# Kernel optimization log

Measured on AMD Instinct MI355X. Metric: run time of the kernel, lower is better.

The kernel has to match this reference:

```python
import jax, jax.numpy as jnp
import numpy as np

U, M, E, EL, H, F, C = 200000, 100000, 2000000, 500000, 64, 20, 7


def setup_inputs() -> dict:
    key = jax.random.key(0)
    ks = jax.random.split(key, 20)
    s = 0.02
    return {
        "user_node_id": jnp.arange(U, dtype=jnp.int64),
        "movie_node_id": jnp.arange(M, dtype=jnp.int64),
        "movie_x": jax.random.normal(ks[0], (M, F), jnp.float32),
        "edge_src": jax.random.randint(ks[1], (E,), 0, U),
        "edge_dst": jax.random.randint(ks[2], (E,), 0, M),
        "el_src": jax.random.randint(ks[3], (EL,), 0, U),
        "el_dst": jax.random.randint(ks[4], (EL,), 0, M),
        "user_emb": jax.random.normal(ks[5], (U, H), jnp.float32) * s,
        "movie_emb": jax.random.normal(ks[6], (M, H), jnp.float32) * s,
        "w_movie": jax.random.normal(ks[7], (F, H), jnp.float32) * s,
        "b_movie": jnp.zeros((H,), jnp.float32),
        "l1_rates_Wl": jax.random.normal(ks[8], (H, H), jnp.float32) * s,
        "l1_rates_bl": jnp.zeros((H,), jnp.float32),
        "l1_rates_Wr": jax.random.normal(ks[9], (H, H), jnp.float32) * s,
        "l1_rev_Wl": jax.random.normal(ks[10], (H, H), jnp.float32) * s,
        "l1_rev_bl": jnp.zeros((H,), jnp.float32),
        "l1_rev_Wr": jax.random.normal(ks[11], (H, H), jnp.float32) * s,
        "l2_rates_Wl": jax.random.normal(ks[12], (H, H), jnp.float32) * s,
        "l2_rates_bl": jnp.zeros((H,), jnp.float32),
        "l2_rates_Wr": jax.random.normal(ks[13], (H, H), jnp.float32) * s,
        "l2_rev_Wl": jax.random.normal(ks[14], (H, H), jnp.float32) * s,
        "l2_rev_bl": jnp.zeros((H,), jnp.float32),
        "l2_rev_Wr": jax.random.normal(ks[15], (H, H), jnp.float32) * s,
        "cls_W": jax.random.normal(ks[16], (2 * H, C), jnp.float32) * s,
        "cls_b": jnp.zeros((C,), jnp.float32),
    }


def _sage(x_src, x_dst, src, dst, n_dst, Wl, bl, Wr):
    # mean-aggregate neighbor messages: gather -> segment_sum -> divide by degree
    msg = x_src[src]                                            # [E, H]
    agg = jax.ops.segment_sum(msg, dst, num_segments=n_dst)     # [n_dst, H]
    deg = jax.ops.segment_sum(jnp.ones((src.shape[0],), x_src.dtype), dst,
                              num_segments=n_dst)
    agg = agg / jnp.maximum(deg, 1.0)[:, None]
    return agg @ Wl + bl + x_dst @ Wr                           # SAGEConv: lin_l(aggr) + lin_r(root)


def reference(user_node_id, movie_node_id, movie_x, edge_src, edge_dst,
              el_src, el_dst, user_emb, movie_emb, w_movie, b_movie,
              l1_rates_Wl, l1_rates_bl, l1_rates_Wr,
              l1_rev_Wl, l1_rev_bl, l1_rev_Wr,
              l2_rates_Wl, l2_rates_bl, l2_rates_Wr,
              l2_rev_Wl, l2_rev_bl, l2_rev_Wr,
              cls_W, cls_b):
    # input projections
    x_user = user_emb[user_node_id]                              # [U, H]
    x_movie = movie_x @ w_movie + b_movie + movie_emb[movie_node_id]  # [M, H]

    # hetero GNN layer 1 (relu)
    u1 = jax.nn.relu(_sage(x_movie, x_user, edge_dst, edge_src, x_user.shape[0],
                           l1_rev_Wl, l1_rev_bl, l1_rev_Wr))
    m1 = jax.nn.relu(_sage(x_user, x_movie, edge_src, edge_dst, x_movie.shape[0],
                           l1_rates_Wl, l1_rates_bl, l1_rates_Wr))
    # hetero GNN layer 2 (no activation)
    u2 = _sage(m1, u1, edge_dst, edge_src, u1.shape[0],
               l2_rev_Wl, l2_rev_bl, l2_rev_Wr)
    m2 = _sage(u1, m1, edge_src, edge_dst, m1.shape[0],
               l2_rates_Wl, l2_rates_bl, l2_rates_Wr)

    # edge classifier over labeled (user, movie) pairs
    edge_feat = jnp.concatenate([u2[el_src], m2[el_dst]], axis=-1)  # [EL, 2H]
    return edge_feat @ cls_W + cls_b                                # [EL, C]
```

## Files before the change

kernel.cpp:

```cpp
#include <hip/hip_runtime.h>
#include <cstdint>
#include <cstddef>

#define H 64
#define C 7
#define F 20
#define BSH 9
#define BSZ 512
#define CH 8192

typedef unsigned short u16;
typedef __attribute__((ext_vector_type(8))) short bf16x8;
typedef __attribute__((ext_vector_type(4))) float f32x4;

static __device__ __forceinline__ int imax(int a, int b) { return a > b ? a : b; }
static __device__ __forceinline__ int imin(int a, int b) { return a < b ? a : b; }

static __device__ __forceinline__ float bf2f(u16 v) {
  union { unsigned u; float f; } x; x.u = ((unsigned)v) << 16; return x.f;
}
static __device__ __forceinline__ u16 f2bf(float f) {
  union { float f; unsigned u; } x; x.f = f;
  unsigned r = x.u + 0x7fffu + ((x.u >> 16) & 1u);
  return (u16)(r >> 16);
}
static __device__ __forceinline__ int pack2bf(float a, float b) {
  return (int)f2bf(a) | ((int)f2bf(b) << 16);
}
static __device__ __forceinline__ float lo16f(unsigned v) {
  union { unsigned u; float f; } x; x.u = v << 16; return x.f;
}
static __device__ __forceinline__ float hi16f(unsigned v) {
  union { unsigned u; float f; } x; x.u = v & 0xffff0000u; return x.f;
}

__global__ __launch_bounds__(256) void k_bhist(const int* __restrict__ esrc,
                                               const int* __restrict__ edst, int E,
                                               int* __restrict__ gcnt_u, int* __restrict__ gcnt_m,
                                               int nbu, int nbm) {
  extern __shared__ int sh[];
  int* hu = sh;
  int* hm = sh + nbu;
  for (int i = threadIdx.x; i < nbu + nbm; i += 256) sh[i] = 0;
  __syncthreads();
  int stride = gridDim.x * 256;
  for (int i = blockIdx.x * 256 + threadIdx.x; i < E; i += stride) {
    atomicAdd(&hu[esrc[i] >> BSH], 1);
    atomicAdd(&hm[edst[i] >> BSH], 1);
  }
  __syncthreads();
  for (int i = threadIdx.x; i < nbu; i += 256) if (hu[i]) atomicAdd(&gcnt_u[i], hu[i]);
  for (int i = threadIdx.x; i < nbm; i += 256) if (hm[i]) atomicAdd(&gcnt_m[i], hm[i]);
}

__global__ __launch_bounds__(256) void k_bscan(const int* __restrict__ gcnt_u,
                                               const int* __restrict__ gcnt_m,
                                               int nbu, int nbm, int E,
                                               int* __restrict__ boff_u, int* __restrict__ boff_m,
                                               int* __restrict__ gcur_u, int* __restrict__ gcur_m) {
  __shared__ int s[1024];
  for (int i = threadIdx.x; i < nbu; i += 256) s[i] = gcnt_u[i];
  for (int i = threadIdx.x; i < nbm; i += 256) s[512 + i] = gcnt_m[i];
  __syncthreads();
  if (threadIdx.x == 0) {
    int r = 0;
    for (int i = 0; i < nbu; ++i) { int v = s[i]; s[i] = r; r += v; }
  }
  if (threadIdx.x == 1) {
    int r = 0;
    for (int i = 0; i < nbm; ++i) { int v = s[512 + i]; s[512 + i] = r; r += v; }
  }
  __syncthreads();
  for (int i = threadIdx.x; i < nbu; i += 256) { boff_u[i] = s[i]; gcur_u[i] = s[i]; }
  for (int i = threadIdx.x; i < nbm; i += 256) { boff_m[i] = s[512 + i]; gcur_m[i] = s[512 + i]; }
  if (threadIdx.x == 0) { boff_u[nbu] = E; boff_m[nbm] = E; }
}

__global__ __launch_bounds__(256) void k_bscat(const int* __restrict__ esrc,
                                               const int* __restrict__ edst, int E,
                                               int* __restrict__ gcur_u, int* __restrict__ gcur_m,
                                               unsigned int* __restrict__ pk_u,
                                               unsigned int* __restrict__ pk_m,
                                               int nbu, int nbm, int nchunks) {
  extern __shared__ int sh2[];
  int dir = (blockIdx.x >= (unsigned)nchunks) ? 1 : 0;
  int chunk = dir ? (blockIdx.x - nchunks) : blockIdx.x;
  const int* key = dir ? edst : esrc;
  const int* pay = dir ? esrc : edst;
  int* gcur = dir ? gcur_m : gcur_u;
  unsigned int* pk = dir ? pk_m : pk_u;
  int nb = dir ? nbm : nbu;
  int* cnt = sh2;
  int* base = sh2 + nb;
  int beg = chunk * CH;
  int end = imin(beg + CH, E);
  for (int i = threadIdx.x; i < nb; i += 256) cnt[i] = 0;
  __syncthreads();
  for (int i = beg + threadIdx.x; i < end; i += 256) atomicAdd(&cnt[key[i] >> BSH], 1);
  __syncthreads();
  for (int i = threadIdx.x; i < nb; i += 256) {
    int c = cnt[i];
    base[i] = c ? atomicAdd(&gcur[i], c) : 0;
    cnt[i] = 0;
  }
  __syncthreads();
  for (int i = beg + threadIdx.x; i < end; i += 256) {
    int k = key[i];
    int b = k >> BSH;
    int r = atomicAdd(&cnt[b], 1);
    pk[base[b] + r] = ((unsigned)(k & (BSZ - 1)) << 18) | (unsigned)pay[i];
  }
}

__global__ __launch_bounds__(512) void k_bbuild(const unsigned int* __restrict__ pk_u,
                                                const unsigned int* __restrict__ pk_m,
                                                const int* __restrict__ boff_u,
                                                const int* __restrict__ boff_m,
                                                int nbu, int nbm, int U_, int M_, int E,
                                                int* __restrict__ csr_u, int* __restrict__ csr_m,
                                                int* __restrict__ off_u, int* __restrict__ off_m) {
  __shared__ int hist[BSZ];
  __shared__ int cur[BSZ];
  int dir = (blockIdx.x >= (unsigned)nbu) ? 1 : 0;
  int b = dir ? (blockIdx.x - nbu) : blockIdx.x;
  const unsigned int* pk = dir ? pk_m : pk_u;
  const int* boff = dir ? boff_m : boff_u;
  int N = dir ? M_ : U_;
  int nb = dir ? nbm : nbu;
  int* csr = dir ? csr_m : csr_u;
  int* off = dir ? off_m : off_u;
  int beg = boff[b], end = boff[b + 1];
  int t = threadIdx.x;
  hist[t] = 0;
  __syncthreads();
  for (int i = beg + t; i < end; i += 512) atomicAdd(&hist[pk[i] >> 18], 1);
  __syncthreads();
  int v0 = hist[t];
  for (int o = 1; o < 512; o <<= 1) {
    int x = (t >= o) ? hist[t - o] : 0;
    __syncthreads();
    hist[t] += x;
    __syncthreads();
  }
  int excl = hist[t] - v0;
  cur[t] = excl;
  int node = (b << BSH) + t;
  if (node < N) off[node] = beg + excl;
  if (t == 0 && b == nb - 1) off[N] = E;
  __syncthreads();
  for (int i = beg + t; i < end; i += 512) {
    unsigned int p = pk[i];
    int n = (int)(p >> 18);
    int r = atomicAdd(&cur[n], 1);
    csr[beg + r] = (int)(p & 0x3FFFFu);
  }
}

__global__ __launch_bounds__(256) void k_prep(
    const float* __restrict__ movie_x, const float* __restrict__ w_movie,
    const float* __restrict__ b_movie, const float* __restrict__ movie_emb,
    const int* __restrict__ mnid,
    const float* __restrict__ user_emb, const int* __restrict__ unid,
    const float* __restrict__ l2u_Wl, const float* __restrict__ l2u_Wr,
    const float* __restrict__ l2u_bl,
    const float* __restrict__ l2m_Wl, const float* __restrict__ l2m_Wr,
    const float* __restrict__ l2m_bl,
    const float* __restrict__ clsW,
    u16* __restrict__ xm_bf, u16* __restrict__ xu_bf, float* __restrict__ cw,
    int M_, int U_, int gProj, int gCvt) {
  __shared__ float ws_[F * H];
  int b = blockIdx.x;
  if (b < gProj) {
    for (int i = threadIdx.x; i < F * H; i += 256) ws_[i] = w_movie[i];
    __syncthreads();
    int t = b * 256 + threadIdx.x;
    int m = t >> 6;
    int h = t & 63;
    if (m >= M_) return;
    float acc = b_movie[h] + movie_emb[(size_t)mnid[m] * H + h];
    const float* xr = movie_x + (size_t)m * F;
    #pragma unroll
    for (int f = 0; f < F; ++f) acc += xr[f] * ws_[f * H + h];
    xm_bf[(size_t)m * H + h] = f2bf(acc);
  } else if (b < gProj + gCvt) {
    int t = (b - gProj) * 256 + threadIdx.x;
    if (t >= U_ * 16) return;
    int i = t >> 4;
    int g = t & 15;
    const float4 v = *(const float4*)(user_emb + (size_t)unid[i] * H + g * 4);
    ushort4 o;
    o.x = f2bf(v.x); o.y = f2bf(v.y); o.z = f2bf(v.z); o.w = f2bf(v.w);
    *(ushort4*)(xu_bf + (size_t)i * H + g * 4) = o;
  } else {
    int t = (b - gProj - gCvt) * 256 + threadIdx.x;
    if (t < 448) {
      int k = t / C, c = t % C;
      float s = 0.f;
      for (int j = 0; j < H; ++j) s += l2u_Wl[k * H + j] * clsW[j * C + c];
      cw[t] = s;
    } else if (t < 896) {
      int u = t - 448; int k = u / C, c = u % C;
      float s = 0.f;
      for (int j = 0; j < H; ++j) s += l2u_Wr[k * H + j] * clsW[j * C + c];
      cw[t] = s;
    } else if (t < 1344) {
      int u = t - 896; int k = u / C, c = u % C;
      float s = 0.f;
      for (int j = 0; j < H; ++j) s += l2m_Wl[k * H + j] * clsW[(H + j) * C + c];
      cw[t] = s;
    } else if (t < 1792) {
      int u = t - 1344; int k = u / C, c = u % C;
      float s = 0.f;
      for (int j = 0; j < H; ++j) s += l2m_Wr[k * H + j] * clsW[(H + j) * C + c];
      cw[t] = s;
    } else if (t < 1799) {
      int c = t - 1792;
      float s = 0.f;
      for (int j = 0; j < H; ++j) s += l2u_bl[j] * clsW[j * C + c];
      cw[t] = s;
    } else if (t < 1806) {
      int c = t - 1799;
      float s = 0.f;
      for (int j = 0; j < H; ++j) s += l2m_bl[j] * clsW[(H + j) * C + c];
      cw[t] = s;
    }
  }
}

__global__ __launch_bounds__(512, 4) void k_sage_mfma(
    const u16* __restrict__ xu, const u16* __restrict__ xm,
    const int* __restrict__ csr_u, const int* __restrict__ off_u,
    const int* __restrict__ csr_m, const int* __restrict__ off_m,
    const float* __restrict__ WlU, const float* __restrict__ blU, const float* __restrict__ WrU,
    const float* __restrict__ WlM, const float* __restrict__ blM, const float* __restrict__ WrM,
    const float* __restrict__ CWml, const float* __restrict__ CWur,
    const float* __restrict__ CWul, const float* __restrict__ CWmr,
    u16* __restrict__ Zu, u16* __restrict__ Zm,
    int U_, int M_, int E_, int gU) {
  __shared__ int sWl[64 * 36];
  __shared__ int sWr[64 * 36];
  __shared__ int sAggHi[128 * 36];
  __shared__ int sAggLo[128 * 36];
  __shared__ float sCl[448];
  __shared__ float sCr[448];
  __shared__ float sBl[64];

  int movie = (blockIdx.x >= (unsigned)gU) ? 1 : 0;
  int bside = movie ? (blockIdx.x - gU) : blockIdx.x;
  const u16* srcT = movie ? xu : xm;
  const u16* rootT = movie ? xm : xu;
  const int* csr = movie ? csr_m : csr_u;
  const int* off = movie ? off_m : off_u;
  const float* Wl = movie ? WlM : WlU;
  const float* Wr = movie ? WrM : WrU;
  const float* bl = movie ? blM : blU;
  const float* CWl = movie ? CWul : CWml;
  const float* CWr = movie ? CWmr : CWur;
  u16* Z = movie ? Zm : Zu;
  int N = movie ? M_ : U_;

  int tid = threadIdx.x;
  for (int idx = tid; idx < 2048; idx += 512) {
    int j = idx & 63, kk = idx >> 6;
    sWl[j * 36 + kk] = pack2bf(Wl[(2 * kk) * H + j], Wl[(2 * kk + 1) * H + j]);
    sWr[j * 36 + kk] = pack2bf(Wr[(2 * kk) * H + j], Wr[(2 * kk + 1) * H + j]);
  }
  for (int idx = tid; idx < 448; idx += 512) { sCl[idx] = CWl[idx]; sCr[idx] = CWr[idx]; }
  if (tid < 64) sBl[tid] = bl[tid];
  __syncthreads();

  int lane = tid & 63;
  int wid = tid >> 6;
  int slot = lane >> 3;
  int l3 = lane & 7;
  int sbase = slot * 8;
  int node0 = bside * 128 + wid * 16;

  #pragma unroll
  for (int g = 0; g < 2; ++g) {
    int n = node0 + g * 8 + slot;
    int nc = n < N ? n : N - 1;
    int jb = off[nc];
    int d = off[nc + 1] - jb;
    if (n >= N) d = 0;
    int dm1 = imax(d - 1, 0);
    int dmax = d;
    dmax = imax(dmax, __shfl_xor(dmax, 8));
    dmax = imax(dmax, __shfl_xor(dmax, 16));
    dmax = imax(dmax, __shfl_xor(dmax, 32));

    float acc[8] = {0.f, 0.f, 0.f, 0.f, 0.f, 0.f, 0.f, 0.f};
    for (int tb = 0; tb < dmax; tb += 8) {
      int ci = jb + imin(tb + l3, dm1);
      ci = imin(ci, E_ - 1);
      int e = csr[ci];
      uint4 v[8];
      #pragma unroll
      for (int k = 0; k < 8; ++k) {
        int a = __shfl(e, sbase + k);
        v[k] = *(const uint4*)(srcT + (size_t)(unsigned)a * H + l3 * 8);
      }
      #pragma unroll
      for (int k = 0; k < 8; ++k) {
        float mk = (tb + k < d) ? 1.0f : 0.0f;
        acc[0] = fmaf(lo16f(v[k].x), mk, acc[0]);
        acc[1] = fmaf(hi16f(v[k].x), mk, acc[1]);
        acc[2] = fmaf(lo16f(v[k].y), mk, acc[2]);
        acc[3] = fmaf(hi16f(v[k].y), mk, acc[3]);
        acc[4] = fmaf(lo16f(v[k].z), mk, acc[4]);
        acc[5] = fmaf(hi16f(v[k].z), mk, acc[5]);
        acc[6] = fmaf(lo16f(v[k].w), mk, acc[6]);
        acc[7] = fmaf(hi16f(v[k].w), mk, acc[7]);
      }
    }

    float inv = 1.0f / (float)imax(d, 1);
    int hi4[4], lo4[4];
    #pragma unroll
    for (int pp = 0; pp < 4; ++pp) {
      float s0 = acc[2 * pp] * inv;
      float s1 = acc[2 * pp + 1] * inv;
      u16 b0 = f2bf(s0), b1 = f2bf(s1);
      float r0 = s0 - bf2f(b0), r1 = s1 - bf2f(b1);
      hi4[pp] = (int)b0 | ((int)b1 << 16);
      lo4[pp] = pack2bf(r0, r1);
    }
    int row = wid * 16 + g * 8 + slot;
    *(int4*)&sAggHi[row * 36 + l3 * 4] = *(int4*)hi4;
    *(int4*)&sAggLo[row * 36 + l3 * 4] = *(int4*)lo4;
  }

  int r16 = lane & 15;
  int q4 = lane >> 4;
  union FU { int4 i; bf16x8 b; };
  FU ahi[2], alo[2], art[2];
  int arow = wid * 16 + r16;
  int rnode = node0 + r16;
  rnode = rnode < N ? rnode : N - 1;
  #pragma unroll
  for (int kt = 0; kt < 2; ++kt) {
    ahi[kt].i = *(const int4*)&sAggHi[arow * 36 + kt * 16 + q4 * 4];
    alo[kt].i = *(const int4*)&sAggLo[arow * 36 + kt * 16 + q4 * 4];
    art[kt].i = ((const int4*)(rootT + (size_t)rnode * H))[kt * 4 + q4];
  }
  float val[4][4];
  #pragma unroll
  for (int t = 0; t < 4; ++t) {
    f32x4 cacc = {0.f, 0.f, 0.f, 0.f};
    #pragma unroll
    for (int kt = 0; kt < 2; ++kt) {
      FU bwl, bwr;
      bwl.i = *(const int4*)&sWl[(t * 16 + r16) * 36 + kt * 16 + q4 * 4];
      bwr.i = *(const int4*)&sWr[(t * 16 + r16) * 36 + kt * 16 + q4 * 4];
      cacc = __builtin_amdgcn_mfma_f32_16x16x32_bf16(ahi[kt].b, bwl.b, cacc, 0, 0, 0);
      cacc = __builtin_amdgcn_mfma_f32_16x16x32_bf16(alo[kt].b, bwl.b, cacc, 0, 0, 0);
      cacc = __builtin_amdgcn_mfma_f32_16x16x32_bf16(art[kt].b, bwr.b, cacc, 0, 0, 0);
    }
    float bj = sBl[t * 16 + r16];
    #pragma unroll
    for (int r = 0; r < 4; ++r) val[t][r] = fmaxf(cacc[r] + bj, 0.f);
  }

  float zacc[4] = {0.f, 0.f, 0.f, 0.f};
  #pragma unroll
  for (int c = 0; c < C; ++c) {
    float tl[4], tr[4];
    #pragma unroll
    for (int r = 0; r < 4; ++r) {
      tl[r] = val[0][r] * sCl[(r16) * C + c] + val[1][r] * sCl[(16 + r16) * C + c] +
              val[2][r] * sCl[(32 + r16) * C + c] + val[3][r] * sCl[(48 + r16) * C + c];
      tr[r] = val[0][r] * sCr[(r16) * C + c] + val[1][r] * sCr[(16 + r16) * C + c] +
              val[2][r] * sCr[(32 + r16) * C + c] + val[3][r] * sCr[(48 + r16) * C + c];
    }
    #pragma unroll
    for (int o = 1; o < 16; o <<= 1) {
      #pragma unroll
      for (int r = 0; r < 4; ++r) {
        tl[r] += __shfl_xor(tl[r], o);
        tr[r] += __shfl_xor(tr[r], o);
      }
    }
    #pragma unroll
    for (int r = 0; r < 4; ++r) {
      zacc[r] = (r16 == c) ? zacc[r] + tl[r] : zacc[r];
      zacc[r] = (r16 == 8 + c) ? zacc[r] + tr[r] : zacc[r];
    }
  }
  #pragma unroll
  for (int r = 0; r < 4; ++r) {
    int node = node0 + q4 * 4 + r;
    if (node < N) Z[(size_t)node * 16 + r16] = f2bf(zacc[r]);
  }
}

__global__ __launch_bounds__(256) void k_agg7m(
    const u16* __restrict__ Zu, const u16* __restrict__ Zm,
    const int* __restrict__ csr_u, const int* __restrict__ off_u,
    const int* __restrict__ csr_m, const int* __restrict__ off_m,
    const float* __restrict__ cbu, const float* __restrict__ cbm,
    float* __restrict__ Pu, float* __restrict__ Pm,
    int U_, int M_, int gU) {
  int movie = (blockIdx.x >= (unsigned)gU) ? 1 : 0;
  int bside = movie ? (blockIdx.x - gU) : blockIdx.x;
  const u16* Zsrc = movie ? Zu : Zm;
  const u16* Zroot = movie ? Zm : Zu;
  const int* csr = movie ? csr_m : csr_u;
  const int* off = movie ? off_m : off_u;
  const float* cb = movie ? cbm : cbu;
  float* P = movie ? Pm : Pu;
  int N = movie ? M_ : U_;

  int n = bside * 256 + threadIdx.x;
  if (n >= N) return;
  int beg = off[n], end = off[n + 1];
  float acc[8] = {0.f, 0.f, 0.f, 0.f, 0.f, 0.f, 0.f, 0.f};
  for (int j = beg; j < end; ++j) {
    int a = csr[j];
    uint4 z = *(const uint4*)(Zsrc + (size_t)a * 16);
    acc[0] += lo16f(z.x); acc[1] += hi16f(z.x);
    acc[2] += lo16f(z.y); acc[3] += hi16f(z.y);
    acc[4] += lo16f(z.z); acc[5] += hi16f(z.z);
    acc[6] += lo16f(z.w); acc[7] += hi16f(z.w);
  }
  float inv = 1.f / (float)imax(end - beg, 1);
  uint4 zr = *(const uint4*)(Zroot + (size_t)n * 16 + 8);
  float4 o0, o1;
  o0.x = acc[0] * inv + lo16f(zr.x) + cb[0];
  o0.y = acc[1] * inv + hi16f(zr.x) + cb[1];
  o0.z = acc[2] * inv + lo16f(zr.y) + cb[2];
  o0.w = acc[3] * inv + hi16f(zr.y) + cb[3];
  o1.x = acc[4] * inv + lo16f(zr.z) + cb[4];
  o1.y = acc[5] * inv + hi16f(zr.z) + cb[5];
  o1.z = acc[6] * inv + lo16f(zr.w) + cb[6];
  o1.w = 0.f;
  float4* po = (float4*)(P + (size_t)n * 8);
  po[0] = o0;
  po[1] = o1;
}

__global__ void k_final(const int* __restrict__ els, const int* __restrict__ eld,
                        const float* __restrict__ Pu, const float* __restrict__ Pm,
                        const float* __restrict__ clsb, float* __restrict__ out, int total) {
  int t = blockIdx.x * 256 + threadIdx.x;
  if (t >= total) return;
  int e = t / C, c = t - e * C;
  out[t] = Pu[(size_t)els[e] * 8 + c] + Pm[(size_t)eld[e] * 8 + c] + clsb[c];
}

extern "C" void kernel_launch(void* const* d_in, const int* in_sizes, int n_in,
                              void* d_out, int out_size, void* d_ws, size_t ws_size,
                              hipStream_t stream) {
  (void)n_in; (void)out_size; (void)ws_size;
  const int*   unid      = (const int*)d_in[0];
  const int*   mnid      = (const int*)d_in[1];
  const float* movie_x   = (const float*)d_in[2];
  const int*   e_src     = (const int*)d_in[3];
  const int*   e_dst     = (const int*)d_in[4];
  const int*   el_src    = (const int*)d_in[5];
  const int*   el_dst    = (const int*)d_in[6];
  const float* user_emb  = (const float*)d_in[7];
  const float* movie_emb = (const float*)d_in[8];
  const float* w_movie   = (const float*)d_in[9];
  const float* b_movie   = (const float*)d_in[10];
  const float* l1r_Wl    = (const float*)d_in[11];
  const float* l1r_bl    = (const float*)d_in[12];
  const float* l1r_Wr    = (const float*)d_in[13];
  const float* l1v_Wl    = (const float*)d_in[14];
  const float* l1v_bl    = (const float*)d_in[15];
  const float* l1v_Wr    = (const float*)d_in[16];
  const float* l2r_Wl    = (const float*)d_in[17];
  const float* l2r_bl    = (const float*)d_in[18];
  const float* l2r_Wr    = (const float*)d_in[19];
  const float* l2v_Wl    = (const float*)d_in[20];
  const float* l2v_bl    = (const float*)d_in[21];
  const float* l2v_Wr    = (const float*)d_in[22];
  const float* cls_W     = (const float*)d_in[23];
  const float* cls_b     = (const float*)d_in[24];

  int U  = in_sizes[0];
  int M  = in_sizes[1];
  int E  = in_sizes[3];
  int EL = in_sizes[5];

  int nbu = (U + BSZ - 1) / BSZ;
  int nbm = (M + BSZ - 1) / BSZ;
  int nchunks = (E + CH - 1) / CH;

  char* p = (char*)d_ws;
  auto alloc = [&](size_t nbytes) { char* r = p; p += (nbytes + 255) & ~(size_t)255; return r; };

  u16*   xm_bf  = (u16*)alloc((size_t)M * H * 2);
  u16*   xu_bf  = (u16*)alloc((size_t)U * H * 2);
  u16*   Zu     = (u16*)alloc((size_t)U * 16 * 2);
  u16*   Zm     = (u16*)alloc((size_t)M * 16 * 2);
  float* Pu     = (float*)alloc((size_t)U * 8 * 4);
  float* Pm     = (float*)alloc((size_t)M * 8 * 4);
  int*   csr_u  = (int*)alloc((size_t)E * 4);
  int*   csr_m  = (int*)alloc((size_t)E * 4);
  int*   off_u  = (int*)alloc((size_t)(U + 1) * 4);
  int*   off_m  = (int*)alloc((size_t)(M + 1) * 4);
  unsigned int* pk_u = (unsigned int*)alloc((size_t)E * 4);
  unsigned int* pk_m = (unsigned int*)alloc((size_t)E * 4);
  int*   gcnt   = (int*)alloc((size_t)(nbu + nbm) * 4);
  int*   gcnt_u = gcnt;
  int*   gcnt_m = gcnt + nbu;
  int*   boff_u = (int*)alloc((size_t)(nbu + 1) * 4);
  int*   boff_m = (int*)alloc((size_t)(nbm + 1) * 4);
  int*   gcur_u = (int*)alloc((size_t)nbu * 4);
  int*   gcur_m = (int*)alloc((size_t)nbm * 4);
  float* cw     = (float*)alloc(1806 * 4);
  float* CWul = cw, *CWur = cw + 448, *CWml = cw + 896, *CWmr = cw + 1344;
  float* cbu  = cw + 1792, *cbm = cw + 1799;

  hipMemsetAsync(gcnt, 0, (size_t)(nbu + nbm) * 4, stream);

  k_bhist<<<256, 256, (size_t)(nbu + nbm) * 4, stream>>>(e_src, e_dst, E, gcnt_u, gcnt_m, nbu, nbm);
  k_bscan<<<1, 256, 0, stream>>>(gcnt_u, gcnt_m, nbu, nbm, E, boff_u, boff_m, gcur_u, gcur_m);
  k_bscat<<<2 * nchunks, 256, (size_t)(2 * nbu) * 4, stream>>>(e_src, e_dst, E, gcur_u, gcur_m,
                                                               pk_u, pk_m, nbu, nbm, nchunks);
  k_bbuild<<<nbu + nbm, 512, 0, stream>>>(pk_u, pk_m, boff_u, boff_m, nbu, nbm, U, M, E,
                                          csr_u, csr_m, off_u, off_m);

  int gProj = (M * H + 255) / 256;
  int gCvt  = (U * 16 + 255) / 256;
  k_prep<<<gProj + gCvt + 8, 256, 0, stream>>>(
      movie_x, w_movie, b_movie, movie_emb, mnid, user_emb, unid,
      l2v_Wl, l2v_Wr, l2v_bl, l2r_Wl, l2r_Wr, l2r_bl, cls_W,
      xm_bf, xu_bf, cw, M, U, gProj, gCvt);

  int gU_s = (U + 127) / 128;
  int gM_s = (M + 127) / 128;
  k_sage_mfma<<<gU_s + gM_s, 512, 0, stream>>>(
      xu_bf, xm_bf, csr_u, off_u, csr_m, off_m,
      l1v_Wl, l1v_bl, l1v_Wr,
      l1r_Wl, l1r_bl, l1r_Wr,
      CWml, CWur, CWul, CWmr,
      Zu, Zm, U, M, E, gU_s);

  int gU_a = (U + 255) / 256;
  int gM_a = (M + 255) / 256;
  k_agg7m<<<gU_a + gM_a, 256, 0, stream>>>(Zu, Zm, csr_u, off_u, csr_m, off_m,
                                           cbu, cbm, Pu, Pm, U, M, gU_a);

  int total = EL * C;
  k_final<<<(total + 255) / 256, 256, 0, stream>>>(el_src, el_dst, Pu, Pm, cls_b, (float*)d_out, total);
}
```

Baseline: 524.6 us.

## Gather neighbors directly in MFMA operand layout, drop LDS staging buffers

```diff
diff --git a/kernel.cpp b/kernel.cpp
--- a/kernel.cpp
+++ b/kernel.cpp
@@ -227,7 +227,7 @@
   }
 }
 
-__global__ __launch_bounds__(512, 4) void k_sage_mfma(
+__global__ __launch_bounds__(256, 6) void k_sage_mfma(
     const u16* __restrict__ xu, const u16* __restrict__ xm,
     const int* __restrict__ csr_u, const int* __restrict__ off_u,
     const int* __restrict__ csr_m, const int* __restrict__ off_m,
@@ -239,8 +239,6 @@
     int U_, int M_, int E_, int gU) {
   __shared__ int sWl[64 * 36];
   __shared__ int sWr[64 * 36];
-  __shared__ int sAggHi[128 * 36];
-  __shared__ int sAggLo[128 * 36];
   __shared__ float sCl[448];
   __shared__ float sCr[448];
   __shared__ float sBl[64];
@@ -260,89 +258,97 @@
   int N = movie ? M_ : U_;
 
   int tid = threadIdx.x;
-  for (int idx = tid; idx < 2048; idx += 512) {
+  for (int idx = tid; idx < 2048; idx += 256) {
     int j = idx & 63, kk = idx >> 6;
     sWl[j * 36 + kk] = pack2bf(Wl[(2 * kk) * H + j], Wl[(2 * kk + 1) * H + j]);
     sWr[j * 36 + kk] = pack2bf(Wr[(2 * kk) * H + j], Wr[(2 * kk + 1) * H + j]);
   }
-  for (int idx = tid; idx < 448; idx += 512) { sCl[idx] = CWl[idx]; sCr[idx] = CWr[idx]; }
+  for (int idx = tid; idx < 448; idx += 256) { sCl[idx] = CWl[idx]; sCr[idx] = CWr[idx]; }
   if (tid < 64) sBl[tid] = bl[tid];
   __syncthreads();
 
   int lane = tid & 63;
   int wid = tid >> 6;
-  int slot = lane >> 3;
-  int l3 = lane & 7;
-  int sbase = slot * 8;
-  int node0 = bside * 128 + wid * 16;
-
-  #pragma unroll
-  for (int g = 0; g < 2; ++g) {
-    int n = node0 + g * 8 + slot;
-    int nc = n < N ? n : N - 1;
-    int jb = off[nc];
-    int d = off[nc + 1] - jb;
-    if (n >= N) d = 0;
-    int dm1 = imax(d - 1, 0);
-    int dmax = d;
-    dmax = imax(dmax, __shfl_xor(dmax, 8));
-    dmax = imax(dmax, __shfl_xor(dmax, 16));
-    dmax = imax(dmax, __shfl_xor(dmax, 32));
-
-    float acc[8] = {0.f, 0.f, 0.f, 0.f, 0.f, 0.f, 0.f, 0.f};
-    for (int tb = 0; tb < dmax; tb += 8) {
-      int ci = jb + imin(tb + l3, dm1);
-      ci = imin(ci, E_ - 1);
-      int e = csr[ci];
-      uint4 v[8];
-      #pragma unroll
-      for (int k = 0; k < 8; ++k) {
-        int a = __shfl(e, sbase + k);
-        v[k] = *(const uint4*)(srcT + (size_t)(unsigned)a * H + l3 * 8);
-      }
-      #pragma unroll
-      for (int k = 0; k < 8; ++k) {
-        float mk = (tb + k < d) ? 1.0f : 0.0f;
-        acc[0] = fmaf(lo16f(v[k].x), mk, acc[0]);
-        acc[1] = fmaf(hi16f(v[k].x), mk, acc[1]);
-        acc[2] = fmaf(lo16f(v[k].y), mk, acc[2]);
-        acc[3] = fmaf(hi16f(v[k].y), mk, acc[3]);
-        acc[4] = fmaf(lo16f(v[k].z), mk, acc[4]);
-        acc[5] = fmaf(hi16f(v[k].z), mk, acc[5]);
-        acc[6] = fmaf(lo16f(v[k].w), mk, acc[6]);
-        acc[7] = fmaf(hi16f(v[k].w), mk, acc[7]);
-      }
-    }
-
-    float inv = 1.0f / (float)imax(d, 1);
-    int hi4[4], lo4[4];
-    #pragma unroll
-    for (int pp = 0; pp < 4; ++pp) {
-      float s0 = acc[2 * pp] * inv;
-      float s1 = acc[2 * pp + 1] * inv;
-      u16 b0 = f2bf(s0), b1 = f2bf(s1);
-      float r0 = s0 - bf2f(b0), r1 = s1 - bf2f(b1);
-      hi4[pp] = (int)b0 | ((int)b1 << 16);
-      lo4[pp] = pack2bf(r0, r1);
-    }
-    int row = wid * 16 + g * 8 + slot;
-    *(int4*)&sAggHi[row * 36 + l3 * 4] = *(int4*)hi4;
-    *(int4*)&sAggLo[row * 36 + l3 * 4] = *(int4*)lo4;
-  }
-
   int r16 = lane & 15;
   int q4 = lane >> 4;
+  int node0 = bside * 64 + wid * 16;
+  int n = node0 + r16;
+  int nc = imin(n, N - 1);
+  int jb = off[nc];
+  int d = off[nc + 1] - jb;
+  if (n >= N) d = 0;
+  int dm1 = imax(d - 1, 0);
+  int Em1 = E_ - 1;
+
+  int dmax = d;
+  dmax = imax(dmax, __shfl_xor(dmax, 1));
+  dmax = imax(dmax, __shfl_xor(dmax, 2));
+  dmax = imax(dmax, __shfl_xor(dmax, 4));
+  dmax = imax(dmax, __shfl_xor(dmax, 8));
+
+  const u16* sb = srcT + q4 * 8;
+  float a0c[8] = {0.f, 0.f, 0.f, 0.f, 0.f, 0.f, 0.f, 0.f};
+  float a1c[8] = {0.f, 0.f, 0.f, 0.f, 0.f, 0.f, 0.f, 0.f};
+
+  for (int t = 0; t < dmax; t += 2) {
+    int c0 = imin(jb + imin(t, dm1), Em1);
+    int c1 = imin(jb + imin(t + 1, dm1), Em1);
+    int e0 = csr[c0];
+    int e1 = csr[c1];
+    const u16* p0 = sb + (size_t)(unsigned)e0 * H;
+    const u16* p1 = sb + (size_t)(unsigned)e1 * H;
+    uint4 v00 = *(const uint4*)p0;
+    uint4 v01 = *(const uint4*)(p0 + 32);
+    uint4 v10 = *(const uint4*)p1;
+    uint4 v11 = *(const uint4*)(p1 + 32);
+    float m0 = (t < d) ? 1.0f : 0.0f;
+    float m1 = (t + 1 < d) ? 1.0f : 0.0f;
+    a0c[0] = fmaf(lo16f(v00.x), m0, a0c[0]); a0c[1] = fmaf(hi16f(v00.x), m0, a0c[1]);
+    a0c[2] = fmaf(lo16f(v00.y), m0, a0c[2]); a0c[3] = fmaf(hi16f(v00.y), m0, a0c[3]);
+    a0c[4] = fmaf(lo16f(v00.z), m0, a0c[4]); a0c[5] = fmaf(hi16f(v00.z), m0, a0c[5]);
+    a0c[6] = fmaf(lo16f(v00.w), m0, a0c[6]); a0c[7] = fmaf(hi16f(v00.w), m0, a0c[7]);
+    a1c[0] = fmaf(lo16f(v01.x), m0, a1c[0]); a1c[1] = fmaf(hi16f(v01.x), m0, a1c[1]);
+    a1c[2] = fmaf(lo16f(v01.y), m0, a1c[2]); a1c[3] = fmaf(hi16f(v01.y), m0, a1c[3]);
+    a1c[4] = fmaf(lo16f(v01.z), m0, a1c[4]); a1c[5] = fmaf(hi16f(v01.z), m0, a1c[5]);
+    a1c[6] = fmaf(lo16f(v01.w), m0, a1c[6]); a1c[7] = fmaf(hi16f(v01.w), m0, a1c[7]);
+    a0c[0] = fmaf(lo16f(v10.x), m1, a0c[0]); a0c[1] = fmaf(hi16f(v10.x), m1, a0c[1]);
+    a0c[2] = fmaf(lo16f(v10.y), m1, a0c[2]); a0c[3] = fmaf(hi16f(v10.y), m1, a0c[3]);
+    a0c[4] = fmaf(lo16f(v10.z), m1, a0c[4]); a0c[5] = fmaf(hi16f(v10.z), m1, a0c[5]);
+    a0c[6] = fmaf(lo16f(v10.w), m1, a0c[6]); a0c[7] = fmaf(hi16f(v10.w), m1, a0c[7]);
+    a1c[0] = fmaf(lo16f(v11.x), m1, a1c[0]); a1c[1] = fmaf(hi16f(v11.x), m1, a1c[1]);
+    a1c[2] = fmaf(lo16f(v11.y), m1, a1c[2]); a1c[3] = fmaf(hi16f(v11.y), m1, a1c[3]);
+    a1c[4] = fmaf(lo16f(v11.z), m1, a1c[4]); a1c[5] = fmaf(hi16f(v11.z), m1, a1c[5]);
+    a1c[6] = fmaf(lo16f(v11.w), m1, a1c[6]); a1c[7] = fmaf(hi16f(v11.w), m1, a1c[7]);
+  }
+
   union FU { int4 i; bf16x8 b; };
   FU ahi[2], alo[2], art[2];
-  int arow = wid * 16 + r16;
-  int rnode = node0 + r16;
-  rnode = rnode < N ? rnode : N - 1;
+  float inv = 1.0f / (float)imax(d, 1);
+  {
+    int h4[4], l4[4];
+    #pragma unroll
+    for (int pp = 0; pp < 4; ++pp) {
+      float s0 = a0c[2 * pp] * inv, s1 = a0c[2 * pp + 1] * inv;
+      u16 b0 = f2bf(s0), b1 = f2bf(s1);
+      h4[pp] = (int)b0 | ((int)b1 << 16);
+      l4[pp] = pack2bf(s0 - bf2f(b0), s1 - bf2f(b1));
+    }
+    ahi[0].i = make_int4(h4[0], h4[1], h4[2], h4[3]);
+    alo[0].i = make_int4(l4[0], l4[1], l4[2], l4[3]);
+    #pragma unroll
+    for (int pp = 0; pp < 4; ++pp) {
+      float s0 = a1c[2 * pp] * inv, s1 = a1c[2 * pp + 1] * inv;
+      u16 b0 = f2bf(s0), b1 = f2bf(s1);
+      h4[pp] = (int)b0 | ((int)b1 << 16);
+      l4[pp] = pack2bf(s0 - bf2f(b0), s1 - bf2f(b1));
+    }
+    ahi[1].i = make_int4(h4[0], h4[1], h4[2], h4[3]);
+    alo[1].i = make_int4(l4[0], l4[1], l4[2], l4[3]);
+  }
   #pragma unroll
-  for (int kt = 0; kt < 2; ++kt) {
-    ahi[kt].i = *(const int4*)&sAggHi[arow * 36 + kt * 16 + q4 * 4];
-    alo[kt].i = *(const int4*)&sAggLo[arow * 36 + kt * 16 + q4 * 4];
-    art[kt].i = ((const int4*)(rootT + (size_t)rnode * H))[kt * 4 + q4];
-  }
+  for (int kt = 0; kt < 2; ++kt)
+    art[kt].i = *(const int4*)(rootT + (size_t)nc * H + kt * 32 + q4 * 8);
+
   float val[4][4];
   #pragma unroll
   for (int t = 0; t < 4; ++t) {
@@ -414,13 +420,27 @@
   if (n >= N) return;
   int beg = off[n], end = off[n + 1];
   float acc[8] = {0.f, 0.f, 0.f, 0.f, 0.f, 0.f, 0.f, 0.f};
-  for (int j = beg; j < end; ++j) {
-    int a = csr[j];
-    uint4 z = *(const uint4*)(Zsrc + (size_t)a * 16);
-    acc[0] += lo16f(z.x); acc[1] += hi16f(z.x);
-    acc[2] += lo16f(z.y); acc[3] += hi16f(z.y);
-    acc[4] += lo16f(z.z); acc[5] += hi16f(z.z);
-    acc[6] += lo16f(z.w); acc[7] += hi16f(z.w);
+  int j = beg;
+  for (; j + 2 <= end; j += 2) {
+    int a0 = csr[j], a1 = csr[j + 1];
+    uint4 z0 = *(const uint4*)(Zsrc + (size_t)a0 * 16);
+    uint4 z1 = *(const uint4*)(Zsrc + (size_t)a1 * 16);
+    acc[0] += lo16f(z0.x); acc[1] += hi16f(z0.x);
+    acc[2] += lo16f(z0.y); acc[3] += hi16f(z0.y);
+    acc[4] += lo16f(z0.z); acc[5] += hi16f(z0.z);
+    acc[6] += lo16f(z0.w); acc[7] += hi16f(z0.w);
+    acc[0] += lo16f(z1.x); acc[1] += hi16f(z1.x);
+    acc[2] += lo16f(z1.y); acc[3] += hi16f(z1.y);
+    acc[4] += lo16f(z1.z); acc[5] += hi16f(z1.z);
+    acc[6] += lo16f(z1.w); acc[7] += hi16f(z1.w);
+  }
+  if (j < end) {
+    int a0 = csr[j];
+    uint4 z0 = *(const uint4*)(Zsrc + (size_t)a0 * 16);
+    acc[0] += lo16f(z0.x); acc[1] += hi16f(z0.x);
+    acc[2] += lo16f(z0.y); acc[3] += hi16f(z0.y);
+    acc[4] += lo16f(z0.z); acc[5] += hi16f(z0.z);
+    acc[6] += lo16f(z0.w); acc[7] += hi16f(z0.w);
   }
   float inv = 1.f / (float)imax(end - beg, 1);
   uint4 zr = *(const uint4*)(Zroot + (size_t)n * 16 + 8);
@@ -528,9 +548,9 @@
       l2v_Wl, l2v_Wr, l2v_bl, l2r_Wl, l2r_Wr, l2r_bl, cls_W,
       xm_bf, xu_bf, cw, M, U, gProj, gCvt);
 
-  int gU_s = (U + 127) / 128;
-  int gM_s = (M + 127) / 128;
-  k_sage_mfma<<<gU_s + gM_s, 512, 0, stream>>>(
+  int gU_s = (U + 63) / 64;
+  int gM_s = (M + 63) / 64;
+  k_sage_mfma<<<gU_s + gM_s, 256, 0, stream>>>(
       xu_bf, xm_bf, csr_u, off_u, csr_m, off_m,
       l1v_Wl, l1v_bl, l1v_Wr,
       l1r_Wl, l1r_bl, l1r_Wr,
```

New measurement: 584.3 us. 11.4% more time.
